# Optimization experiments

Hardware: AMD Instinct MI355X
Metric: run time of the kernel (lower is better)

## Reference

```python
import jax, jax.numpy as jnp
import numpy as np


def setup_inputs() -> dict:
    key = jax.random.key(0)
    k1, k2, k3 = jax.random.split(key, 3)
    B, H, G, L, S, D = 2, 8, 4, 2048, 2048, 128
    q = jax.random.normal(k1, (B, H, G, L, D), dtype=jnp.float32)
    k = jax.random.normal(k2, (B, H, 1, S, D), dtype=jnp.float32)
    v = jax.random.normal(k3, (B, H, 1, S, D), dtype=jnp.float32)
    return {"q": q, "k": k, "v": v}


def reference(q, k, v):
    # q: [B,H,G,L,D]; k,v: [B,H,1,S,D] broadcast over G groups.
    # NOTE: original module does NOT scale by 1/sqrt(D).
    kk = jnp.squeeze(k, axis=2)  # [B,H,S,D]
    vv = jnp.squeeze(v, axis=2)  # [B,H,S,D]
    scores = jnp.einsum('bhgld,bhsd->bhgls', q, kk)  # [B,H,G,L,S]
    probs = jax.nn.softmax(scores, axis=-1)
    return jnp.einsum('bhgls,bhsd->bhgld', probs, vv)  # [B,H,G,L,D]
```

## Files before the change

kernel.cpp:

```cpp
#include <hip/hip_runtime.h>
#include <hip/hip_bf16.h>
#include <math.h>

typedef __bf16 bf16x8 __attribute__((ext_vector_type(8)));
typedef __bf16 bf16x4 __attribute__((ext_vector_type(4)));
typedef float  f32x4  __attribute__((ext_vector_type(4)));

constexpr int D   = 128;
constexpr int LQ  = 2048;
constexpr int SK  = 2048;
constexpr int BM  = 256;
constexpr int BN  = 64;
constexpr int NKV = 16;
constexpr int NT  = SK / BN;

__device__ __forceinline__ void load_lds16(const void* g, void* l) {
  __builtin_amdgcn_global_load_lds((const __attribute__((address_space(1))) unsigned*)g,
                                   (__attribute__((address_space(3))) unsigned*)l, 16, 0, 0);
}

__device__ __forceinline__ f32x4 vmax4(f32x4 a, f32x4 b) {
  f32x4 r;
  r[0] = fmaxf(a[0], b[0]); r[1] = fmaxf(a[1], b[1]);
  r[2] = fmaxf(a[2], b[2]); r[3] = fmaxf(a[3], b[3]);
  return r;
}

__global__ __launch_bounds__(256) void conv_k(const float* __restrict__ k,
                                              __bf16* __restrict__ khi,
                                              __bf16* __restrict__ klo) {
  const size_t i = ((size_t)blockIdx.x * 256 + threadIdx.x) * 4;
  f32x4 a = *(const f32x4*)(k + i);
  bf16x4 hi, lo;
#pragma unroll
  for (int j = 0; j < 4; ++j) {
    hi[j] = (__bf16)a[j];
    lo[j] = (__bf16)(a[j] - (float)hi[j]);
  }
  *(bf16x4*)(khi + i) = hi;
  *(bf16x4*)(klo + i) = lo;
}

__global__ __launch_bounds__(256) void transpose_v(const float* __restrict__ v,
                                                   __bf16* __restrict__ vt) {
  const int b    = blockIdx.x;
  const int bh   = b >> 6;
  const int t2   = (b & 63) * 256 + threadIdx.x;
  const int d    = t2 & 127;
  const int slot = t2 >> 7;
  const int G    = slot >> 1;
  const int h2   = slot & 1;
  const float* src = v + ((size_t)bh * SK + 32 * G) * D + d;
  bf16x8 o0, o1;
#pragma unroll
  for (int qq = 0; qq < 2; ++qq)
#pragma unroll
    for (int h = 0; h < 2; ++h)
#pragma unroll
      for (int r = 0; r < 4; ++r) {
        const int idx = 8 * qq + 4 * h + r;
        const int w   = 16 * h + 4 * (2 * h2 + qq) + r;
        const __bf16 val = (__bf16)src[(size_t)w * D];
        if (idx < 8) o0[idx] = val; else o1[idx - 8] = val;
      }
  __bf16* dst = vt + ((size_t)bh * D + d) * SK + 32 * G + 16 * h2;
  *(bf16x8*)dst = o0;
  *(bf16x8*)(dst + 8) = o1;
}

__global__ __launch_bounds__(512, 2)
void gqa_fwd(const float* __restrict__ qg, const __bf16* __restrict__ khi_g,
             const __bf16* __restrict__ klo_g, const __bf16* __restrict__ vt_g,
             float* __restrict__ outg)
{
  __shared__ alignas(16) __bf16 Kh[2][BN * D];
  __shared__ alignas(16) __bf16 Kl[2][BN * D];
  __shared__ alignas(16) __bf16 Vs[3][D * BN];

  const int bid   = blockIdx.x;
  const int xcd   = bid & 7;
  const int idx   = bid >> 3;
  const int bh    = 2 * xcd + (idx & 1);
  const int grp   = (idx >> 1) & 3;
  const int qtile = idx >> 3;
  const int bhg   = bh * 4 + grp;

  const int tid  = threadIdx.x;
  const int wave = tid >> 6;
  const int lane = tid & 63;
  const int i16  = lane & 15;
  const int quad = lane >> 4;

  const float*  qbase = qg + (size_t)bhg * (LQ * D) + (size_t)(qtile * BM) * D;
  const __bf16* khb   = khi_g + (size_t)bh * (SK * D);
  const __bf16* klb   = klo_g + (size_t)bh * (SK * D);
  const __bf16* vtb   = vt_g + (size_t)bh * (D * SK);

  auto stage_k = [&](int s0, int buf) {
#pragma unroll
    for (int c = 0; c < 2; ++c) {
      const int wc   = 2 * wave + c;
      const int srow = wc * 4 + (lane >> 4);
      const int jk   = (lane & 15) ^ (srow & 15);
      load_lds16(khb + (size_t)(s0 + srow) * D + 8 * jk, (char*)&Kh[buf][0] + wc * 1024);
      load_lds16(klb + (size_t)(s0 + srow) * D + 8 * jk, (char*)&Kl[buf][0] + wc * 1024);
    }
  };
  auto stage_v = [&](int s0, int slot) {
#pragma unroll
    for (int c = 0; c < 2; ++c) {
      const int wc   = 2 * wave + c;
      const int drow = wc * 8 + (lane >> 3);
      const int jv   = (lane & 7) ^ (drow & 7);
      load_lds16(vtb + (size_t)drow * SK + s0 + 8 * jv, (char*)&Vs[slot][0] + wc * 1024);
    }
  };

  stage_k(0, 0);  stage_v(0, 0);
  stage_k(BN, 1); stage_v(BN, 1);

  constexpr float LOG2E = 1.44269504089f;
  bf16x8 qhi[2][4], qlo[2][4];
#pragma unroll
  for (int u = 0; u < 2; ++u) {
    const float* qp = qbase + (size_t)(32 * wave + 16 * u + i16) * D + 8 * quad;
#pragma unroll
    for (int t = 0; t < 4; ++t) {
      f32x4 a = *(const f32x4*)(qp + 32 * t);
      f32x4 b = *(const f32x4*)(qp + 32 * t + 4);
#pragma unroll
      for (int j = 0; j < 4; ++j) {
        const float a2 = a[j] * LOG2E;
        const float b2 = b[j] * LOG2E;
        qhi[u][t][j]     = (__bf16)a2;
        qlo[u][t][j]     = (__bf16)(a2 - (float)qhi[u][t][j]);
        qhi[u][t][j + 4] = (__bf16)b2;
        qlo[u][t][j + 4] = (__bf16)(b2 - (float)qhi[u][t][j + 4]);
      }
    }
  }

  f32x4 o_acc[2][8];
#pragma unroll
  for (int u = 0; u < 2; ++u)
#pragma unroll
    for (int c = 0; c < 8; ++c) o_acc[u][c] = (f32x4){0.f, 0.f, 0.f, 0.f};
  float m_r[2] = {-INFINITY, -INFINITY};
  float l_r[2] = {0.f, 0.f};

  auto qk_tile = [&](const __bf16* khc, const __bf16* klc, f32x4 (&sf)[2][4]) {
#pragma unroll
    for (int n = 0; n < 4; ++n) {
      sf[0][n] = (f32x4){0.f, 0.f, 0.f, 0.f};
      sf[1][n] = (f32x4){0.f, 0.f, 0.f, 0.f};
    }
#pragma unroll
    for (int n = 0; n < 4; ++n) {
#pragma unroll
      for (int t = 0; t < 4; ++t) {
        const int ke = (16 * n + i16) * 128 + 8 * ((4 * t + quad) ^ i16);
        bf16x8 kh = *(const bf16x8*)&khc[ke];
        bf16x8 kl = *(const bf16x8*)&klc[ke];
#pragma unroll
        for (int u = 0; u < 2; ++u) {
          sf[u][n] = __builtin_amdgcn_mfma_f32_16x16x32_bf16(kh, qhi[u][t], sf[u][n], 0, 0, 0);
          sf[u][n] = __builtin_amdgcn_mfma_f32_16x16x32_bf16(kh, qlo[u][t], sf[u][n], 0, 0, 0);
          sf[u][n] = __builtin_amdgcn_mfma_f32_16x16x32_bf16(kl, qhi[u][t], sf[u][n], 0, 0, 0);
        }
      }
    }
  };
  auto pv_tile = [&](const __bf16* vsc, bf16x8 (&pc)[2][2]) {
#pragma unroll
    for (int c = 0; c < 8; ++c) {
      const int row = 16 * c + i16;
#pragma unroll
      for (int t = 0; t < 2; ++t) {
        bf16x8 av = *(const bf16x8*)&vsc[row * 64 + 8 * ((4 * t + quad) ^ (i16 & 7))];
#pragma unroll
        for (int u = 0; u < 2; ++u)
          o_acc[u][c] = __builtin_amdgcn_mfma_f32_16x16x32_bf16(av, pc[u][t], o_acc[u][c], 0, 0, 0);
      }
    }
  };
  auto softmax_tile = [&](f32x4 (&sf)[2][4], bf16x8 (&pn)[2][2]) {
#pragma unroll
    for (int u = 0; u < 2; ++u) {
      f32x4 vm = vmax4(vmax4(sf[u][0], sf[u][1]), vmax4(sf[u][2], sf[u][3]));
      float mx = fmaxf(fmaxf(vm[0], vm[1]), fmaxf(vm[2], vm[3]));
      mx = fmaxf(mx, __shfl_xor(mx, 16, 64));
      mx = fmaxf(mx, __shfl_xor(mx, 32, 64));
      const float mnew  = fmaxf(m_r[u], mx);
      const float alpha = exp2f(m_r[u] - mnew);
      m_r[u] = mnew;
      f32x4 rs4 = (f32x4){0.f, 0.f, 0.f, 0.f};
#pragma unroll
      for (int t = 0; t < 2; ++t)
#pragma unroll
        for (int h = 0; h < 2; ++h)
#pragma unroll
          for (int r = 0; r < 4; ++r) {
            const float p   = exp2f(sf[2 * 0 + u][2 * t + h][r] - mnew);
            const __bf16 pv = (__bf16)p;
            pn[u][t][4 * h + r] = pv;
            rs4[r] += (float)pv;
          }
      float rs = (rs4[0] + rs4[1]) + (rs4[2] + rs4[3]);
      rs += __shfl_xor(rs, 16, 64);
      rs += __shfl_xor(rs, 32, 64);
      l_r[u] = l_r[u] * alpha + rs;
#pragma unroll
      for (int c = 0; c < 8; ++c) o_acc[u][c] = o_acc[u][c] * alpha;
    }
  };

  asm volatile("s_waitcnt vmcnt(0)" ::: "memory");
  __syncthreads();

  bf16x8 pb_cur[2][2], pb_nxt[2][2];
  {
    f32x4 sf[2][4];
    qk_tile(&Kh[0][0], &Kl[0][0], sf);
    softmax_tile(sf, pb_cur);
  }
  __syncthreads();

  int vcur = 0;
  for (int t = 0; t < NT - 1; ++t) {
    const int s2 = ((t + 2) & (NT - 1)) * BN;
    stage_k(s2, t & 1);
    int vstage = vcur + 2; vstage -= (vstage >= 3) ? 3 : 0;
    stage_v(s2, vstage);

    f32x4 sf[2][4];
    qk_tile(&Kh[(t + 1) & 1][0], &Kl[(t + 1) & 1][0], sf);

    pv_tile(&Vs[vcur][0], pb_cur);

    softmax_tile(sf, pb_nxt);

#pragma unroll
    for (int u = 0; u < 2; ++u)
#pragma unroll
      for (int tt = 0; tt < 2; ++tt) pb_cur[u][tt] = pb_nxt[u][tt];
    vcur += 1; vcur -= (vcur >= 3) ? 3 : 0;

    asm volatile("s_waitcnt vmcnt(0)" ::: "memory");
    __syncthreads();
  }

  pv_tile(&Vs[vcur][0], pb_cur);

  float* obase = outg + (size_t)bhg * (LQ * D) + (size_t)(qtile * BM) * D;
#pragma unroll
  for (int u = 0; u < 2; ++u) {
    const float inv = 1.f / l_r[u];
    float* op = obase + (size_t)(32 * wave + 16 * u + i16) * D;
#pragma unroll
    for (int c = 0; c < 8; ++c) {
      f32x4 r4 = o_acc[u][c] * inv;
      *(f32x4*)(op + 16 * c + 4 * quad) = r4;
    }
  }
}

extern "C" void kernel_launch(void* const* d_in, const int* in_sizes, int n_in,
                              void* d_out, int out_size, void* d_ws, size_t ws_size,
                              hipStream_t stream) {
  const float* q = (const float*)d_in[0];
  const float* k = (const float*)d_in[1];
  const float* v = (const float*)d_in[2];
  float* out = (float*)d_out;
  (void)in_sizes; (void)n_in; (void)out_size; (void)ws_size;

  const size_t kv_elems = (size_t)NKV * SK * D;
  __bf16* khi = (__bf16*)d_ws;
  __bf16* klo = khi + kv_elems;
  __bf16* vt  = klo + kv_elems;

  conv_k<<<dim3(kv_elems / (256 * 4)), 256, 0, stream>>>(k, khi, klo);
  transpose_v<<<dim3(NKV * 64), 256, 0, stream>>>(v, vt);
  gqa_fwd<<<dim3(8 * (LQ / BM) * 8), 512, 0, stream>>>(q, khi, klo, vt, out);
}
```

Measured before the change: 398.5 us.

## Switch attention to fp16 with single-K split and two-term Q split

Replaces the bf16 hi/lo split scheme with fp16. K is stored as a single fp16 array, Q is kept as hi+lo fp16, and V is also fp16. This cuts QK MFMAs from three to two per K fragment, halves K staging traffic and LDS, and shrinks the V ring from three buffers to two. The main loop is unrolled by two with compile-time buffer indices to remove the rotation copies. It trades K precision (fp16 rounding without a low part) and fp16 range limits on P and V for fewer matrix ops and less memory traffic.

After: 384.4 us. 1.04x faster.

```diff
diff --git a/kernel.cpp b/kernel.cpp
--- a/kernel.cpp
+++ b/kernel.cpp
@@ -2,9 +2,9 @@
 #include <hip/hip_bf16.h>
 #include <math.h>
 
-typedef __bf16 bf16x8 __attribute__((ext_vector_type(8)));
-typedef __bf16 bf16x4 __attribute__((ext_vector_type(4)));
-typedef float  f32x4  __attribute__((ext_vector_type(4)));
+typedef _Float16 half8 __attribute__((ext_vector_type(8)));
+typedef _Float16 half4 __attribute__((ext_vector_type(4)));
+typedef float    f32x4 __attribute__((ext_vector_type(4)));
 
 constexpr int D   = 128;
 constexpr int LQ  = 2048;
@@ -14,6 +14,8 @@
 constexpr int NKV = 16;
 constexpr int NT  = SK / BN;
 
+template <int N> struct IC { static constexpr int v = N; };
+
 __device__ __forceinline__ void load_lds16(const void* g, void* l) {
   __builtin_amdgcn_global_load_lds((const __attribute__((address_space(1))) unsigned*)g,
                                    (__attribute__((address_space(3))) unsigned*)l, 16, 0, 0);
@@ -26,23 +28,18 @@
   return r;
 }
 
-__global__ __launch_bounds__(256) void conv_k(const float* __restrict__ k,
-                                              __bf16* __restrict__ khi,
-                                              __bf16* __restrict__ klo) {
+__global__ __launch_bounds__(256) void conv_k16(const float* __restrict__ k,
+                                                _Float16* __restrict__ kh) {
   const size_t i = ((size_t)blockIdx.x * 256 + threadIdx.x) * 4;
   f32x4 a = *(const f32x4*)(k + i);
-  bf16x4 hi, lo;
-#pragma unroll
-  for (int j = 0; j < 4; ++j) {
-    hi[j] = (__bf16)a[j];
-    lo[j] = (__bf16)(a[j] - (float)hi[j]);
-  }
-  *(bf16x4*)(khi + i) = hi;
-  *(bf16x4*)(klo + i) = lo;
+  half4 h;
+#pragma unroll
+  for (int j = 0; j < 4; ++j) h[j] = (_Float16)a[j];
+  *(half4*)(kh + i) = h;
 }
 
 __global__ __launch_bounds__(256) void transpose_v(const float* __restrict__ v,
-                                                   __bf16* __restrict__ vt) {
+                                                   _Float16* __restrict__ vt) {
   const int b    = blockIdx.x;
   const int bh   = b >> 6;
   const int t2   = (b & 63) * 256 + threadIdx.x;
@@ -51,7 +48,7 @@
   const int G    = slot >> 1;
   const int h2   = slot & 1;
   const float* src = v + ((size_t)bh * SK + 32 * G) * D + d;
-  bf16x8 o0, o1;
+  half8 o0, o1;
 #pragma unroll
   for (int qq = 0; qq < 2; ++qq)
 #pragma unroll
@@ -60,22 +57,20 @@
       for (int r = 0; r < 4; ++r) {
         const int idx = 8 * qq + 4 * h + r;
         const int w   = 16 * h + 4 * (2 * h2 + qq) + r;
-        const __bf16 val = (__bf16)src[(size_t)w * D];
+        const _Float16 val = (_Float16)src[(size_t)w * D];
         if (idx < 8) o0[idx] = val; else o1[idx - 8] = val;
       }
-  __bf16* dst = vt + ((size_t)bh * D + d) * SK + 32 * G + 16 * h2;
-  *(bf16x8*)dst = o0;
-  *(bf16x8*)(dst + 8) = o1;
+  _Float16* dst = vt + ((size_t)bh * D + d) * SK + 32 * G + 16 * h2;
+  *(half8*)dst = o0;
+  *(half8*)(dst + 8) = o1;
 }
 
 __global__ __launch_bounds__(512, 2)
-void gqa_fwd(const float* __restrict__ qg, const __bf16* __restrict__ khi_g,
-             const __bf16* __restrict__ klo_g, const __bf16* __restrict__ vt_g,
-             float* __restrict__ outg)
+void gqa_fwd(const float* __restrict__ qg, const _Float16* __restrict__ kh_g,
+             const _Float16* __restrict__ vt_g, float* __restrict__ outg)
 {
-  __shared__ alignas(16) __bf16 Kh[2][BN * D];
-  __shared__ alignas(16) __bf16 Kl[2][BN * D];
-  __shared__ alignas(16) __bf16 Vs[3][D * BN];
+  __shared__ alignas(16) _Float16 Kh[2][BN * D];
+  __shared__ alignas(16) _Float16 Vs[2][D * BN];
 
   const int bid   = blockIdx.x;
   const int xcd   = bid & 7;
@@ -91,36 +86,35 @@
   const int i16  = lane & 15;
   const int quad = lane >> 4;
 
-  const float*  qbase = qg + (size_t)bhg * (LQ * D) + (size_t)(qtile * BM) * D;
-  const __bf16* khb   = khi_g + (size_t)bh * (SK * D);
-  const __bf16* klb   = klo_g + (size_t)bh * (SK * D);
-  const __bf16* vtb   = vt_g + (size_t)bh * (D * SK);
-
-  auto stage_k = [&](int s0, int buf) {
+  const float*    qbase = qg + (size_t)bhg * (LQ * D) + (size_t)(qtile * BM) * D;
+  const _Float16* khb   = kh_g + (size_t)bh * (SK * D);
+  const _Float16* vtb   = vt_g + (size_t)bh * (D * SK);
+
+  auto stage_k = [&](int s0, _Float16* dst) {
 #pragma unroll
     for (int c = 0; c < 2; ++c) {
       const int wc   = 2 * wave + c;
       const int srow = wc * 4 + (lane >> 4);
       const int jk   = (lane & 15) ^ (srow & 15);
-      load_lds16(khb + (size_t)(s0 + srow) * D + 8 * jk, (char*)&Kh[buf][0] + wc * 1024);
-      load_lds16(klb + (size_t)(s0 + srow) * D + 8 * jk, (char*)&Kl[buf][0] + wc * 1024);
-    }
-  };
-  auto stage_v = [&](int s0, int slot) {
+      load_lds16(khb + (size_t)(s0 + srow) * D + 8 * jk, (char*)dst + wc * 1024);
+    }
+  };
+  auto stage_v = [&](int s0, _Float16* dst) {
 #pragma unroll
     for (int c = 0; c < 2; ++c) {
       const int wc   = 2 * wave + c;
       const int drow = wc * 8 + (lane >> 3);
       const int jv   = (lane & 7) ^ (drow & 7);
-      load_lds16(vtb + (size_t)drow * SK + s0 + 8 * jv, (char*)&Vs[slot][0] + wc * 1024);
-    }
-  };
-
-  stage_k(0, 0);  stage_v(0, 0);
-  stage_k(BN, 1); stage_v(BN, 1);
+      load_lds16(vtb + (size_t)drow * SK + s0 + 8 * jv, (char*)dst + wc * 1024);
+    }
+  };
+
+  stage_k(0, &Kh[0][0]);
+  stage_k(BN, &Kh[1][0]);
+  stage_v(0, &Vs[0][0]);
 
   constexpr float LOG2E = 1.44269504089f;
-  bf16x8 qhi[2][4], qlo[2][4];
+  half8 qhi[2][4], qlo[2][4];
 #pragma unroll
   for (int u = 0; u < 2; ++u) {
     const float* qp = qbase + (size_t)(32 * wave + 16 * u + i16) * D + 8 * quad;
@@ -132,10 +126,10 @@
       for (int j = 0; j < 4; ++j) {
         const float a2 = a[j] * LOG2E;
         const float b2 = b[j] * LOG2E;
-        qhi[u][t][j]     = (__bf16)a2;
-        qlo[u][t][j]     = (__bf16)(a2 - (float)qhi[u][t][j]);
-        qhi[u][t][j + 4] = (__bf16)b2;
-        qlo[u][t][j + 4] = (__bf16)(b2 - (float)qhi[u][t][j + 4]);
+        qhi[u][t][j]     = (_Float16)a2;
+        qlo[u][t][j]     = (_Float16)(a2 - (float)qhi[u][t][j]);
+        qhi[u][t][j + 4] = (_Float16)b2;
+        qlo[u][t][j + 4] = (_Float16)(b2 - (float)qhi[u][t][j + 4]);
       }
     }
   }
@@ -148,7 +142,7 @@
   float m_r[2] = {-INFINITY, -INFINITY};
   float l_r[2] = {0.f, 0.f};
 
-  auto qk_tile = [&](const __bf16* khc, const __bf16* klc, f32x4 (&sf)[2][4]) {
+  auto qk_tile = [&](const _Float16* khc, f32x4 (&sf)[2][4]) {
 #pragma unroll
     for (int n = 0; n < 4; ++n) {
       sf[0][n] = (f32x4){0.f, 0.f, 0.f, 0.f};
@@ -159,31 +153,29 @@
 #pragma unroll
       for (int t = 0; t < 4; ++t) {
         const int ke = (16 * n + i16) * 128 + 8 * ((4 * t + quad) ^ i16);
-        bf16x8 kh = *(const bf16x8*)&khc[ke];
-        bf16x8 kl = *(const bf16x8*)&klc[ke];
+        half8 kh = *(const half8*)&khc[ke];
 #pragma unroll
         for (int u = 0; u < 2; ++u) {
-          sf[u][n] = __builtin_amdgcn_mfma_f32_16x16x32_bf16(kh, qhi[u][t], sf[u][n], 0, 0, 0);
-          sf[u][n] = __builtin_amdgcn_mfma_f32_16x16x32_bf16(kh, qlo[u][t], sf[u][n], 0, 0, 0);
-          sf[u][n] = __builtin_amdgcn_mfma_f32_16x16x32_bf16(kl, qhi[u][t], sf[u][n], 0, 0, 0);
+          sf[u][n] = __builtin_amdgcn_mfma_f32_16x16x32_f16(kh, qhi[u][t], sf[u][n], 0, 0, 0);
+          sf[u][n] = __builtin_amdgcn_mfma_f32_16x16x32_f16(kh, qlo[u][t], sf[u][n], 0, 0, 0);
         }
       }
     }
   };
-  auto pv_tile = [&](const __bf16* vsc, bf16x8 (&pc)[2][2]) {
+  auto pv_tile = [&](const _Float16* vsc, half8 (&pc)[2][2]) {
 #pragma unroll
     for (int c = 0; c < 8; ++c) {
       const int row = 16 * c + i16;
 #pragma unroll
       for (int t = 0; t < 2; ++t) {
-        bf16x8 av = *(const bf16x8*)&vsc[row * 64 + 8 * ((4 * t + quad) ^ (i16 & 7))];
+        half8 av = *(const half8*)&vsc[row * 64 + 8 * ((4 * t + quad) ^ (i16 & 7))];
 #pragma unroll
         for (int u = 0; u < 2; ++u)
-          o_acc[u][c] = __builtin_amdgcn_mfma_f32_16x16x32_bf16(av, pc[u][t], o_acc[u][c], 0, 0, 0);
-      }
-    }
-  };
-  auto softmax_tile = [&](f32x4 (&sf)[2][4], bf16x8 (&pn)[2][2]) {
+          o_acc[u][c] = __builtin_amdgcn_mfma_f32_16x16x32_f16(av, pc[u][t], o_acc[u][c], 0, 0, 0);
+      }
+    }
+  };
+  auto softmax_tile = [&](f32x4 (&sf)[2][4], half8 (&pn)[2][2]) {
 #pragma unroll
     for (int u = 0; u < 2; ++u) {
       f32x4 vm = vmax4(vmax4(sf[u][0], sf[u][1]), vmax4(sf[u][2], sf[u][3]));
@@ -200,8 +192,8 @@
         for (int h = 0; h < 2; ++h)
 #pragma unroll
           for (int r = 0; r < 4; ++r) {
-            const float p   = exp2f(sf[2 * 0 + u][2 * t + h][r] - mnew);
-            const __bf16 pv = (__bf16)p;
+            const float p     = exp2f(sf[u][2 * t + h][r] - mnew);
+            const _Float16 pv = (_Float16)p;
             pn[u][t][4 * h + r] = pv;
             rs4[r] += (float)pv;
           }
@@ -217,39 +209,33 @@
   asm volatile("s_waitcnt vmcnt(0)" ::: "memory");
   __syncthreads();
 
-  bf16x8 pb_cur[2][2], pb_nxt[2][2];
+  half8 pbA[2][2], pbB[2][2];
   {
     f32x4 sf[2][4];
-    qk_tile(&Kh[0][0], &Kl[0][0], sf);
-    softmax_tile(sf, pb_cur);
+    qk_tile(&Kh[0][0], sf);
+    softmax_tile(sf, pbA);
   }
   __syncthreads();
 
-  int vcur = 0;
-  for (int t = 0; t < NT - 1; ++t) {
-    const int s2 = ((t + 2) & (NT - 1)) * BN;
-    stage_k(s2, t & 1);
-    int vstage = vcur + 2; vstage -= (vstage >= 3) ? 3 : 0;
-    stage_v(s2, vstage);
-
+  auto body = [&](int t, auto curc, half8 (&pbU)[2][2], half8 (&pbF)[2][2]) {
+    constexpr int CUR = decltype(curc)::v;
+    stage_k(((t + 2) & (NT - 1)) * BN, &Kh[CUR][0]);
+    stage_v((t + 1) * BN, &Vs[CUR ^ 1][0]);
     f32x4 sf[2][4];
-    qk_tile(&Kh[(t + 1) & 1][0], &Kl[(t + 1) & 1][0], sf);
-
-    pv_tile(&Vs[vcur][0], pb_cur);
-
-    softmax_tile(sf, pb_nxt);
-
-#pragma unroll
-    for (int u = 0; u < 2; ++u)
-#pragma unroll
-      for (int tt = 0; tt < 2; ++tt) pb_cur[u][tt] = pb_nxt[u][tt];
-    vcur += 1; vcur -= (vcur >= 3) ? 3 : 0;
-
+    qk_tile(&Kh[CUR ^ 1][0], sf);
+    pv_tile(&Vs[CUR][0], pbU);
+    softmax_tile(sf, pbF);
     asm volatile("s_waitcnt vmcnt(0)" ::: "memory");
     __syncthreads();
-  }
-
-  pv_tile(&Vs[vcur][0], pb_cur);
+  };
+
+  for (int tp = 0; tp < 15; ++tp) {
+    body(2 * tp,     IC<0>{}, pbA, pbB);
+    body(2 * tp + 1, IC<1>{}, pbB, pbA);
+  }
+  body(30, IC<0>{}, pbA, pbB);
+
+  pv_tile(&Vs[1][0], pbB);
 
   float* obase = outg + (size_t)bhg * (LQ * D) + (size_t)(qtile * BM) * D;
 #pragma unroll
@@ -274,11 +260,10 @@
   (void)in_sizes; (void)n_in; (void)out_size; (void)ws_size;
 
   const size_t kv_elems = (size_t)NKV * SK * D;
-  __bf16* khi = (__bf16*)d_ws;
-  __bf16* klo = khi + kv_elems;
-  __bf16* vt  = klo + kv_elems;
-
-  conv_k<<<dim3(kv_elems / (256 * 4)), 256, 0, stream>>>(k, khi, klo);
+  _Float16* kh = (_Float16*)d_ws;
+  _Float16* vt = kh + kv_elems;
+
+  conv_k16<<<dim3(kv_elems / (256 * 4)), 256, 0, stream>>>(k, kh);
   transpose_v<<<dim3(NKV * 64), 256, 0, stream>>>(v, vt);
-  gqa_fwd<<<dim3(8 * (LQ / BM) * 8), 512, 0, stream>>>(q, khi, klo, vt, out);
-}
+  gqa_fwd<<<dim3(8 * (LQ / BM) * 8), 512, 0, stream>>>(q, kh, vt, out);
+}
```
